# Kernel optimization log

Measured on AMD Instinct MI355X. Metric: run time of the kernel, lower is better.

The kernel has to match this reference:

```python
import jax, jax.numpy as jnp
import numpy as np

INPUT_DIM = 1024
OUTPUT_DIM = 1024
NUM_HEADS = 16  # NOTE: torch .split(num_heads) => chunk SIZE = num_heads
N_CHUNKS = OUTPUT_DIM // NUM_HEADS  # 64 effective heads of dim 16
NEG_INF = -1e9


def setup_inputs() -> dict:
    key = jax.random.key(0)
    k1, k2, k3, k4 = jax.random.split(key, 4)
    B, S = 32, 256
    x = jax.random.normal(k1, (B, S, INPUT_DIM), dtype=jnp.float32)
    mask = jnp.ones((B, S), dtype=jnp.float32)
    # xavier-uniform-ish linear weights, torch layout [out, in]
    lim = float(np.sqrt(6.0 / (INPUT_DIM + OUTPUT_DIM)))
    Wq = jax.random.uniform(k2, (OUTPUT_DIM, INPUT_DIM), jnp.float32, -lim, lim)
    Wk = jax.random.uniform(k3, (OUTPUT_DIM, INPUT_DIM), jnp.float32, -lim, lim)
    Wv = jax.random.uniform(k4, (OUTPUT_DIM, INPUT_DIM), jnp.float32, -lim, lim)
    return {"batch_sequence": x, "sequence_mask": mask, "Wq": Wq, "Wk": Wk, "Wv": Wv}


def _split_heads(m):
    # [B,S,D] -> chunks of size NUM_HEADS stacked in dim 0: [C,B,S,H]
    B, S, D = m.shape
    return jnp.transpose(m.reshape(B, S, N_CHUNKS, NUM_HEADS), (2, 0, 1, 3))


def reference(batch_sequence, sequence_mask, Wq, Wk, Wv):
    q = _split_heads(batch_sequence @ Wq.T)  # [C,B,S,H]
    k = _split_heads(batch_sequence @ Wk.T)
    v = _split_heads(batch_sequence @ Wv.T)
    logits = jnp.einsum("cbqh,cbkh->cbqk", q, k) / jnp.sqrt(
        jnp.asarray(OUTPUT_DIM, batch_sequence.dtype)
    )
    mask2d = sequence_mask[:, :, None] * sequence_mask[:, None, :]  # [B,S,S]
    logits = jnp.where(mask2d[None] > 0, logits, NEG_INF)
    w = jax.nn.softmax(logits, axis=-1)
    out = jnp.einsum("cbqk,cbkh->cbqh", w, v)  # [C,B,S,H]
    B, S = batch_sequence.shape[:2]
    return jnp.transpose(out, (1, 2, 0, 3)).reshape(B, S, OUTPUT_DIM)
```

## Files before the change

### kernel.cpp

```cpp
#include <hip/hip_runtime.h>


typedef unsigned short u16;
typedef unsigned int u32;
typedef __attribute__((ext_vector_type(8))) short short8;
typedef __attribute__((ext_vector_type(4))) short short4v;
typedef __attribute__((ext_vector_type(4))) float floatx4;

#if __has_builtin(__builtin_amdgcn_mfma_f32_16x16x16bf16_1k)
#define MFMA16(A, B, C) __builtin_amdgcn_mfma_f32_16x16x16bf16_1k(A, B, C, 0, 0, 0)
#elif __has_builtin(__builtin_amdgcn_mfma_f32_16x16x16_bf16)
#define MFMA16(A, B, C) __builtin_amdgcn_mfma_f32_16x16x16_bf16(A, B, C, 0, 0, 0)
#else
__device__ __forceinline__ floatx4 mfma16_asm(short4v a, short4v b, floatx4 c) {
  floatx4 d;
  asm volatile("v_mfma_f32_16x16x16_bf16 %0, %1, %2, %3"
               : "=v"(d) : "v"(a), "v"(b), "v"(c));
  return d;
}
#define MFMA16(A, B, C) mfma16_asm(A, B, C)
#endif

#if __has_builtin(__builtin_amdgcn_exp2f)
#define EXP2(x) __builtin_amdgcn_exp2f(x)
#else
#define EXP2(x) __expf((x) * 0.6931471805599453f)
#endif

#define QSCALE 0.045084220f

__device__ __forceinline__ u16 f2bf(float f) {
  union { float f; u32 u; } x; x.f = f;
  u32 r = x.u + 0x7fffu + ((x.u >> 16) & 1u);
  return (u16)(r >> 16);
}
__device__ __forceinline__ float bf2f(u16 u) {
  union { u32 u; float f; } x; x.u = ((u32)u) << 16;
  return x.f;
}

__device__ __forceinline__ void gload16(const void* g, void* l) {
  typedef __attribute__((address_space(1))) const unsigned int gq;
  typedef __attribute__((address_space(3))) unsigned int lq;
  __builtin_amdgcn_global_load_lds((gq*)(size_t)g, (lq*)(size_t)l, 16, 0, 0);
}

#define GK 1024
#define QKS 20
#define VTS 264

__global__ __launch_bounds__(256) void cast_all(const float* __restrict__ x,
                                                const float* __restrict__ wq,
                                                const float* __restrict__ wk,
                                                const float* __restrict__ wv,
                                                u16* __restrict__ XB,
                                                u16* __restrict__ WB) {
  int bid = blockIdx.x;
  const float* src; u16* dst; int off;
  if (bid < 8192)       { src = x;  dst = XB;                 off = bid; }
  else if (bid < 9216)  { src = wq; dst = WB;                 off = bid - 8192; }
  else if (bid < 10240) { src = wk; dst = WB + 1024 * 1024;   off = bid - 9216; }
  else                  { src = wv; dst = WB + 2 * 1024 * 1024; off = bid - 10240; }
  int i = (off * 256 + threadIdx.x) * 4;
  float4 v = *(const float4*)(src + i);
  u32 lo = (u32)f2bf(v.x) | ((u32)f2bf(v.y) << 16);
  u32 hi = (u32)f2bf(v.z) | ((u32)f2bf(v.w) << 16);
  uint2 o; o.x = lo; o.y = hi;
  *(uint2*)(dst + i) = o;
}

template <bool MASKED>
__device__ __forceinline__ void attn_loop2(const u16* __restrict__ Ks,
                                           const u16* __restrict__ Vt,
                                           const short4v* bq, const float* mqv,
                                           const float* m_s,
                                           floatx4* oacc, floatx4* lacc,
                                           int col, int quad) {
  const short4v ones = {(short)0x3F80, (short)0x3F80, (short)0x3F80, (short)0x3F80};
#pragma unroll 4
  for (int kt = 0; kt < 16; kt++) {
    const int kb = kt * 16;
    short4v ak = *(const short4v*)(Ks + (kb + col) * QKS + quad * 4);
    short4v av = *(const short4v*)(Vt + col * VTS + kb + quad * 4);
    float mk[4];
    if (MASKED) {
#pragma unroll
      for (int i = 0; i < 4; i++) mk[i] = m_s[kb + quad * 4 + i];
    }
#pragma unroll
    for (int qt = 0; qt < 2; qt++) {
      floatx4 z = {0.f, 0.f, 0.f, 0.f};
      floatx4 st = MFMA16(ak, bq[qt], z);
      float e[4];
#pragma unroll
      for (int i = 0; i < 4; i++) {
        e[i] = EXP2(st[i]);
        if (MASKED) e[i] = (mqv[qt] * mk[i] > 0.f) ? e[i] : 0.f;
      }
      union { u32 u[2]; short4v s; } pk;
      pk.u[0] = __builtin_amdgcn_perm(__float_as_uint(e[1]), __float_as_uint(e[0]), 0x07060302u);
      pk.u[1] = __builtin_amdgcn_perm(__float_as_uint(e[3]), __float_as_uint(e[2]), 0x07060302u);
      lacc[qt] = MFMA16(ones, pk.s, lacc[qt]);
      oacc[qt] = MFMA16(av, pk.s, oacc[qt]);
    }
  }
}

__global__ __launch_bounds__(512, 4) void fused_qkv_attn(const u16* __restrict__ XB,
                                                         const u16* __restrict__ WB,
                                                         const float* __restrict__ mask,
                                                         float* __restrict__ out) {
  __shared__ __align__(16) u16 smem[22528];
  __shared__ float m_s[256];

  const int bid = blockIdx.x;
  const int b = bid & 31;
  const int c0 = (bid >> 5) * 2;
  const int t = threadIdx.x;
  const int wave = t >> 6;
  const int lane = t & 63;
  const int col = lane & 15;
  const int quad = lane >> 4;

  u16* const Xs0 = smem;
  u16* const Xs1 = smem + 8192;
  u16* const Ws0 = smem + 16384;
  u16* const Ws1 = smem + 19456;

  float mv = (t < 256) ? mask[b * 256 + t] : 1.0f;
  if (t < 256) m_s[t] = mv;
  const int allones = __syncthreads_and(mv > 0.f);

  const int rl = lane >> 2;
  const int ch = lane & 3;
  const int sch = ch ^ ((rl >> 1) & 3);

  const size_t xsrc = ((size_t)b * 256 + wave * 32 + rl) * GK + sch * 8;
  const int xdst = wave * 1024;

  size_t wsrc = 0;
  if (wave < 6)
    wsrc = ((size_t)((wave % 3) * 1024 + (c0 + wave / 3) * 16 + rl)) * GK + sch * 8;
  const int wdst = wave * 512;

  floatx4 acc[2][6] = {};

  const int rpos = (quad ^ ((col >> 1) & 3)) * 8;
  const int arow0 = (wave * 32 + col) * 32 + rpos;

  gload16(XB + xsrc, Xs0 + xdst);
  gload16(XB + xsrc + (size_t)16 * GK, Xs0 + xdst + 512);
  if (wave < 6) gload16(WB + wsrc, Ws0 + wdst);

  auto gemm_step = [&](int knext, const u16* Xc, const u16* Wc, u16* Xn, u16* Wn) {
    if (knext >= 0) {
      gload16(XB + xsrc + knext, Xn + xdst);
      gload16(XB + xsrc + (size_t)16 * GK + knext, Xn + xdst + 512);
      if (wave < 6) {
        gload16(WB + wsrc + knext, Wn + wdst);
        asm volatile("s_waitcnt vmcnt(3)" ::: "memory");
      } else {
        asm volatile("s_waitcnt vmcnt(2)" ::: "memory");
      }
    } else {
      asm volatile("s_waitcnt vmcnt(0)" ::: "memory");
    }
    __builtin_amdgcn_sched_barrier(0);
    __builtin_amdgcn_s_barrier();
    __builtin_amdgcn_sched_barrier(0);

    short8 af[2], bf[6];
#pragma unroll
    for (int mt = 0; mt < 2; mt++)
      af[mt] = *(const short8*)(Xc + arow0 + mt * 512);
#pragma unroll
    for (int nt = 0; nt < 6; nt++)
      bf[nt] = *(const short8*)(Wc + (nt * 16 + col) * 32 + rpos);
#pragma unroll
    for (int mt = 0; mt < 2; mt++)
#pragma unroll
      for (int nt = 0; nt < 6; nt++)
        acc[mt][nt] = __builtin_amdgcn_mfma_f32_16x16x32_bf16(af[mt], bf[nt], acc[mt][nt], 0, 0, 0);

    asm volatile("s_waitcnt lgkmcnt(0)" ::: "memory");
    __builtin_amdgcn_sched_barrier(0);
    __builtin_amdgcn_s_barrier();
  };

#pragma unroll 1
  for (int tp = 0; tp < 15; tp++) {
    gemm_step((2 * tp + 1) * 32, Xs0, Ws0, Xs1, Ws1);
    gemm_step((2 * tp + 2) * 32, Xs1, Ws1, Xs0, Ws0);
  }
  gemm_step(31 * 32, Xs0, Ws0, Xs1, Ws1);
  gemm_step(-1, Xs1, Ws1, Xs0, Ws0);

  u16* const Qs = smem;
  u16* const Ks = smem + 5120;
  u16* const Vt = smem + 10240;
  float* const l_s = (float*)(smem + 14464);
  float* const ot = (float*)smem;

#pragma unroll
  for (int h = 0; h < 2; h++) {
    __syncthreads();

#pragma unroll
    for (int mt = 0; mt < 2; mt++) {
      const int row = wave * 32 + mt * 16 + quad * 4;
#pragma unroll
      for (int r = 0; r < 4; r++) {
        Qs[(row + r) * QKS + col] = f2bf(acc[mt][3 * h + 0][r] * QSCALE);
        Ks[(row + r) * QKS + col] = f2bf(acc[mt][3 * h + 1][r]);
        Vt[col * VTS + row + r] = f2bf(acc[mt][3 * h + 2][r]);
      }
    }
    __syncthreads();

    const int q0 = wave * 32;
    short4v bq[2];
    float mqv[2];
#pragma unroll
    for (int qt = 0; qt < 2; qt++) {
      bq[qt] = *(const short4v*)(Qs + (q0 + qt * 16 + col) * QKS + quad * 4);
      mqv[qt] = m_s[q0 + qt * 16 + col];
    }

    floatx4 oacc[2] = {};
    floatx4 lacc[2] = {};
    if (allones)
      attn_loop2<false>(Ks, Vt, bq, mqv, m_s, oacc, lacc, col, quad);
    else
      attn_loop2<true>(Ks, Vt, bq, mqv, m_s, oacc, lacc, col, quad);

    __syncthreads();
#pragma unroll
    for (int qt = 0; qt < 2; qt++) {
      if (quad == 0) l_s[q0 + qt * 16 + col] = lacc[qt][0];
#pragma unroll
      for (int r = 0; r < 4; r++)
        ot[(quad * 4 + r) * 257 + q0 + qt * 16 + col] = oacc[qt][r];
    }
    __syncthreads();

    const int row = t >> 1;
    const int hb = (t & 1) * 8;
    float l = l_s[row];
    float* op = out + ((size_t)b * 256 + row) * 1024 + (c0 + h) * 16 + hb;
    float o[8];
    if (allones || l > 0.f) {
      float inv = 1.0f / l;
#pragma unroll
      for (int j = 0; j < 8; j++) o[j] = ot[(hb + j) * 257 + row] * inv;
    } else {
#pragma unroll
      for (int j = 0; j < 8; j++) o[j] = 0.f;
      for (int k = 0; k < 256; k++)
#pragma unroll
        for (int j = 0; j < 8; j++) o[j] += bf2f(Vt[(hb + j) * VTS + k]);
#pragma unroll
      for (int j = 0; j < 8; j++) o[j] *= (1.0f / 256.0f);
    }
#pragma unroll
    for (int g = 0; g < 2; g++) {
      float4 r;
      r.x = o[g * 4 + 0]; r.y = o[g * 4 + 1]; r.z = o[g * 4 + 2]; r.w = o[g * 4 + 3];
      *(float4*)(op + g * 4) = r;
    }
  }
}

extern "C" void kernel_launch(void* const* d_in, const int* in_sizes, int n_in,
                              void* d_out, int out_size, void* d_ws, size_t ws_size,
                              hipStream_t stream) {
  const float* x    = (const float*)d_in[0];
  const float* mask = (const float*)d_in[1];
  const float* Wq   = (const float*)d_in[2];
  const float* Wk   = (const float*)d_in[3];
  const float* Wv   = (const float*)d_in[4];
  float* out = (float*)d_out;

  u16* XB = (u16*)d_ws;
  u16* WB = XB + (size_t)8192 * 1024;

  cast_all<<<11264, 256, 0, stream>>>(x, Wq, Wk, Wv, XB, WB);
  fused_qkv_attn<<<1024, 512, 0, stream>>>(XB, WB, mask, out);
}
```

Measured before the change: 167.5 us.

## Fuse x bf16 cast into attention GEMM and process four heads per block

Drops the separate pass that cast x to bf16. The fused kernel now loads fp32 x straight from global memory, converts it in registers with v_cvt_pk_bf16_f32, and writes it to LDS, so x is no longer written and re-read as bf16 through a workspace. Blocks grow to 1024 threads and handle four heads each, which halves the grid and halves how many times x is re-read across head groups. The waves are re-tiled 4x4 over rows and weights, and each wave now handles 16 queries in the attention phase. The trade-offs are register-staged x loads that are only partly overlapped with the MFMAs, more LDS, and a larger block that may lower occupancy.

```diff
diff --git a/kernel.cpp b/kernel.cpp
--- a/kernel.cpp
+++ b/kernel.cpp
@@ -39,6 +39,12 @@
   return x.f;
 }
 
+__device__ __forceinline__ u32 pkbf(float lo, float hi) {
+  u32 d;
+  asm("v_cvt_pk_bf16_f32 %0, %1, %2" : "=v"(d) : "v"(lo), "v"(hi));
+  return d;
+}
+
 __device__ __forceinline__ void gload16(const void* g, void* l) {
   typedef __attribute__((address_space(1))) const unsigned int gq;
   typedef __attribute__((address_space(3))) unsigned int lq;
@@ -49,32 +55,27 @@
 #define QKS 20
 #define VTS 264
 
-__global__ __launch_bounds__(256) void cast_all(const float* __restrict__ x,
-                                                const float* __restrict__ wq,
-                                                const float* __restrict__ wk,
-                                                const float* __restrict__ wv,
-                                                u16* __restrict__ XB,
-                                                u16* __restrict__ WB) {
+__global__ __launch_bounds__(256) void cast_w(const float* __restrict__ wq,
+                                              const float* __restrict__ wk,
+                                              const float* __restrict__ wv,
+                                              u16* __restrict__ WB) {
   int bid = blockIdx.x;
-  const float* src; u16* dst; int off;
-  if (bid < 8192)       { src = x;  dst = XB;                 off = bid; }
-  else if (bid < 9216)  { src = wq; dst = WB;                 off = bid - 8192; }
-  else if (bid < 10240) { src = wk; dst = WB + 1024 * 1024;   off = bid - 9216; }
-  else                  { src = wv; dst = WB + 2 * 1024 * 1024; off = bid - 10240; }
-  int i = (off * 256 + threadIdx.x) * 4;
+  const float* src = (bid < 1024) ? wq : (bid < 2048) ? wk : wv;
+  int seg = bid >> 10;
+  int i = ((bid & 1023) * 256 + threadIdx.x) * 4;
   float4 v = *(const float4*)(src + i);
-  u32 lo = (u32)f2bf(v.x) | ((u32)f2bf(v.y) << 16);
-  u32 hi = (u32)f2bf(v.z) | ((u32)f2bf(v.w) << 16);
-  uint2 o; o.x = lo; o.y = hi;
-  *(uint2*)(dst + i) = o;
+  uint2 o;
+  o.x = pkbf(v.x, v.y);
+  o.y = pkbf(v.z, v.w);
+  *(uint2*)(WB + (size_t)seg * 1024 * 1024 + i) = o;
 }
 
 template <bool MASKED>
-__device__ __forceinline__ void attn_loop2(const u16* __restrict__ Ks,
+__device__ __forceinline__ void attn_loop1(const u16* __restrict__ Ks,
                                            const u16* __restrict__ Vt,
-                                           const short4v* bq, const float* mqv,
+                                           short4v bq, float mqv,
                                            const float* m_s,
-                                           floatx4* oacc, floatx4* lacc,
+                                           floatx4& oacc, floatx4& lacc,
                                            int col, int quad) {
   const short4v ones = {(short)0x3F80, (short)0x3F80, (short)0x3F80, (short)0x3F80};
 #pragma unroll 4
@@ -82,118 +83,125 @@
     const int kb = kt * 16;
     short4v ak = *(const short4v*)(Ks + (kb + col) * QKS + quad * 4);
     short4v av = *(const short4v*)(Vt + col * VTS + kb + quad * 4);
-    float mk[4];
-    if (MASKED) {
-#pragma unroll
-      for (int i = 0; i < 4; i++) mk[i] = m_s[kb + quad * 4 + i];
-    }
-#pragma unroll
-    for (int qt = 0; qt < 2; qt++) {
-      floatx4 z = {0.f, 0.f, 0.f, 0.f};
-      floatx4 st = MFMA16(ak, bq[qt], z);
-      float e[4];
-#pragma unroll
-      for (int i = 0; i < 4; i++) {
-        e[i] = EXP2(st[i]);
-        if (MASKED) e[i] = (mqv[qt] * mk[i] > 0.f) ? e[i] : 0.f;
-      }
-      union { u32 u[2]; short4v s; } pk;
-      pk.u[0] = __builtin_amdgcn_perm(__float_as_uint(e[1]), __float_as_uint(e[0]), 0x07060302u);
-      pk.u[1] = __builtin_amdgcn_perm(__float_as_uint(e[3]), __float_as_uint(e[2]), 0x07060302u);
-      lacc[qt] = MFMA16(ones, pk.s, lacc[qt]);
-      oacc[qt] = MFMA16(av, pk.s, oacc[qt]);
-    }
-  }
-}
-
-__global__ __launch_bounds__(512, 4) void fused_qkv_attn(const u16* __restrict__ XB,
-                                                         const u16* __restrict__ WB,
-                                                         const float* __restrict__ mask,
-                                                         float* __restrict__ out) {
-  __shared__ __align__(16) u16 smem[22528];
+    floatx4 z = {0.f, 0.f, 0.f, 0.f};
+    floatx4 st = MFMA16(ak, bq, z);
+    float e[4];
+#pragma unroll
+    for (int i = 0; i < 4; i++) {
+      e[i] = EXP2(st[i]);
+      if (MASKED) e[i] = (mqv * m_s[kb + quad * 4 + i] > 0.f) ? e[i] : 0.f;
+    }
+    union { u32 u[2]; short4v s; } pk;
+    pk.u[0] = __builtin_amdgcn_perm(__float_as_uint(e[1]), __float_as_uint(e[0]), 0x07060302u);
+    pk.u[1] = __builtin_amdgcn_perm(__float_as_uint(e[3]), __float_as_uint(e[2]), 0x07060302u);
+    lacc = MFMA16(ones, pk.s, lacc);
+    oacc = MFMA16(av, pk.s, oacc);
+  }
+}
+
+__global__ __launch_bounds__(1024, 4) void fused_qkv_attn(const float* __restrict__ x,
+                                                          const u16* __restrict__ WB,
+                                                          const float* __restrict__ mask,
+                                                          float* __restrict__ out) {
+  __shared__ __align__(16) u16 smem[28672];
   __shared__ float m_s[256];
 
   const int bid = blockIdx.x;
   const int b = bid & 31;
-  const int c0 = (bid >> 5) * 2;
+  const int c0 = (bid >> 5) * 4;
   const int t = threadIdx.x;
   const int wave = t >> 6;
   const int lane = t & 63;
   const int col = lane & 15;
   const int quad = lane >> 4;
+  const int wm = wave & 3;
+  const int wn = wave >> 2;
 
   u16* const Xs0 = smem;
   u16* const Xs1 = smem + 8192;
-  u16* const Ws0 = smem + 16384;
-  u16* const Ws1 = smem + 19456;
+  u16* const WsA = smem + 16384;
+  u16* const WsB = smem + 22528;
 
   float mv = (t < 256) ? mask[b * 256 + t] : 1.0f;
   if (t < 256) m_s[t] = mv;
   const int allones = __syncthreads_and(mv > 0.f);
 
-  const int rl = lane >> 2;
-  const int ch = lane & 3;
-  const int sch = ch ^ ((rl >> 1) & 3);
-
-  const size_t xsrc = ((size_t)b * 256 + wave * 32 + rl) * GK + sch * 8;
-  const int xdst = wave * 1024;
-
+  const int xr = t >> 2;
+  const int xch = t & 3;
+  const float* const xg = x + ((size_t)b * 256 + xr) * GK + xch * 8;
+  const int xdst = xr * 32 + (xch ^ ((xr >> 1) & 3)) * 8;
+
+  const int wr = lane >> 2;
+  const int wch = lane & 3;
+  const int wsch = wch ^ ((wr >> 1) & 3);
   size_t wsrc = 0;
-  if (wave < 6)
-    wsrc = ((size_t)((wave % 3) * 1024 + (c0 + wave / 3) * 16 + rl)) * GK + sch * 8;
+  if (wave < 12) {
+    const int mat = wave % 3, head = wave / 3;
+    wsrc = ((size_t)(mat * 1024 + (c0 + head) * 16 + wr)) * GK + wsch * 8;
+  }
   const int wdst = wave * 512;
 
-  floatx4 acc[2][6] = {};
+  floatx4 acc[4][3] = {};
 
   const int rpos = (quad ^ ((col >> 1) & 3)) * 8;
-  const int arow0 = (wave * 32 + col) * 32 + rpos;
-
-  gload16(XB + xsrc, Xs0 + xdst);
-  gload16(XB + xsrc + (size_t)16 * GK, Xs0 + xdst + 512);
-  if (wave < 6) gload16(WB + wsrc, Ws0 + wdst);
+  const int abase = (wm * 64 + col) * 32 + rpos;
+  const int bbase = (wn * 48 + col) * 32 + rpos;
+
+  if (wave < 12) gload16(WB + wsrc, WsA + wdst);
+  {
+    float4 a0 = *(const float4*)(xg);
+    float4 a1 = *(const float4*)(xg + 4);
+    asm volatile("s_waitcnt vmcnt(0)" ::: "memory");
+    uint4 w;
+    w.x = pkbf(a0.x, a0.y); w.y = pkbf(a0.z, a0.w);
+    w.z = pkbf(a1.x, a1.y); w.w = pkbf(a1.z, a1.w);
+    *(uint4*)(Xs0 + xdst) = w;
+  }
+  asm volatile("s_waitcnt lgkmcnt(0)" ::: "memory");
+  __builtin_amdgcn_sched_barrier(0);
+  __builtin_amdgcn_s_barrier();
+  __builtin_amdgcn_sched_barrier(0);
 
   auto gemm_step = [&](int knext, const u16* Xc, const u16* Wc, u16* Xn, u16* Wn) {
+    float4 a0, a1;
     if (knext >= 0) {
-      gload16(XB + xsrc + knext, Xn + xdst);
-      gload16(XB + xsrc + (size_t)16 * GK + knext, Xn + xdst + 512);
-      if (wave < 6) {
-        gload16(WB + wsrc + knext, Wn + wdst);
-        asm volatile("s_waitcnt vmcnt(3)" ::: "memory");
-      } else {
-        asm volatile("s_waitcnt vmcnt(2)" ::: "memory");
-      }
-    } else {
+      if (wave < 12) gload16(WB + wsrc + knext, Wn + wdst);
+      a0 = *(const float4*)(xg + knext);
+      a1 = *(const float4*)(xg + knext + 4);
+    }
+    __builtin_amdgcn_sched_barrier(0);
+
+    short8 af[4], bf[3];
+#pragma unroll
+    for (int mt = 0; mt < 4; mt++)
+      af[mt] = *(const short8*)(Xc + abase + mt * 512);
+#pragma unroll
+    for (int n = 0; n < 3; n++)
+      bf[n] = *(const short8*)(Wc + bbase + n * 512);
+#pragma unroll
+    for (int mt = 0; mt < 4; mt++)
+#pragma unroll
+      for (int n = 0; n < 3; n++)
+        acc[mt][n] = __builtin_amdgcn_mfma_f32_16x16x32_bf16(af[mt], bf[n], acc[mt][n], 0, 0, 0);
+
+    if (knext >= 0) {
       asm volatile("s_waitcnt vmcnt(0)" ::: "memory");
-    }
+      uint4 w;
+      w.x = pkbf(a0.x, a0.y); w.y = pkbf(a0.z, a0.w);
+      w.z = pkbf(a1.x, a1.y); w.w = pkbf(a1.z, a1.w);
+      *(uint4*)(Xn + xdst) = w;
+    }
+    asm volatile("s_waitcnt lgkmcnt(0)" ::: "memory");
     __builtin_amdgcn_sched_barrier(0);
     __builtin_amdgcn_s_barrier();
     __builtin_amdgcn_sched_barrier(0);
-
-    short8 af[2], bf[6];
-#pragma unroll
-    for (int mt = 0; mt < 2; mt++)
-      af[mt] = *(const short8*)(Xc + arow0 + mt * 512);
-#pragma unroll
-    for (int nt = 0; nt < 6; nt++)
-      bf[nt] = *(const short8*)(Wc + (nt * 16 + col) * 32 + rpos);
-#pragma unroll
-    for (int mt = 0; mt < 2; mt++)
-#pragma unroll
-      for (int nt = 0; nt < 6; nt++)
-        acc[mt][nt] = __builtin_amdgcn_mfma_f32_16x16x32_bf16(af[mt], bf[nt], acc[mt][nt], 0, 0, 0);
-
-    asm volatile("s_waitcnt lgkmcnt(0)" ::: "memory");
-    __builtin_amdgcn_sched_barrier(0);
-    __builtin_amdgcn_s_barrier();
   };
 
 #pragma unroll 1
-  for (int tp = 0; tp < 15; tp++) {
-    gemm_step((2 * tp + 1) * 32, Xs0, Ws0, Xs1, Ws1);
-    gemm_step((2 * tp + 2) * 32, Xs1, Ws1, Xs0, Ws0);
-  }
-  gemm_step(31 * 32, Xs0, Ws0, Xs1, Ws1);
-  gemm_step(-1, Xs1, Ws1, Xs0, Ws0);
+  for (int tp = 0; tp < 16; tp++) {
+    gemm_step((2 * tp + 1) * 32, Xs0, WsA, Xs1, WsB);
+    gemm_step((tp == 15) ? -1 : (2 * tp + 2) * 32, Xs1, WsB, Xs0, WsA);
+  }
 
   u16* const Qs = smem;
   u16* const Ks = smem + 5120;
@@ -202,71 +210,61 @@
   float* const ot = (float*)smem;
 
 #pragma unroll
-  for (int h = 0; h < 2; h++) {
-    __syncthreads();
-
-#pragma unroll
-    for (int mt = 0; mt < 2; mt++) {
-      const int row = wave * 32 + mt * 16 + quad * 4;
-#pragma unroll
-      for (int r = 0; r < 4; r++) {
-        Qs[(row + r) * QKS + col] = f2bf(acc[mt][3 * h + 0][r] * QSCALE);
-        Ks[(row + r) * QKS + col] = f2bf(acc[mt][3 * h + 1][r]);
-        Vt[col * VTS + row + r] = f2bf(acc[mt][3 * h + 2][r]);
+  for (int h = 0; h < 4; h++) {
+    __syncthreads();
+
+    if (wn == h) {
+#pragma unroll
+      for (int mt = 0; mt < 4; mt++) {
+        const int row = wm * 64 + mt * 16 + quad * 4;
+#pragma unroll
+        for (int r = 0; r < 4; r++) {
+          Qs[(row + r) * QKS + col] = f2bf(acc[mt][0][r] * QSCALE);
+          Ks[(row + r) * QKS + col] = f2bf(acc[mt][1][r]);
+          Vt[col * VTS + row + r] = f2bf(acc[mt][2][r]);
+        }
       }
     }
     __syncthreads();
 
-    const int q0 = wave * 32;
-    short4v bq[2];
-    float mqv[2];
-#pragma unroll
-    for (int qt = 0; qt < 2; qt++) {
-      bq[qt] = *(const short4v*)(Qs + (q0 + qt * 16 + col) * QKS + quad * 4);
-      mqv[qt] = m_s[q0 + qt * 16 + col];
-    }
-
-    floatx4 oacc[2] = {};
-    floatx4 lacc[2] = {};
+    const int q0 = wave * 16;
+    short4v bq = *(const short4v*)(Qs + (q0 + col) * QKS + quad * 4);
+    float mqv = m_s[q0 + col];
+    floatx4 oacc = {};
+    floatx4 lacc = {};
     if (allones)
-      attn_loop2<false>(Ks, Vt, bq, mqv, m_s, oacc, lacc, col, quad);
+      attn_loop1<false>(Ks, Vt, bq, mqv, m_s, oacc, lacc, col, quad);
     else
-      attn_loop2<true>(Ks, Vt, bq, mqv, m_s, oacc, lacc, col, quad);
-
-    __syncthreads();
-#pragma unroll
-    for (int qt = 0; qt < 2; qt++) {
-      if (quad == 0) l_s[q0 + qt * 16 + col] = lacc[qt][0];
-#pragma unroll
-      for (int r = 0; r < 4; r++)
-        ot[(quad * 4 + r) * 257 + q0 + qt * 16 + col] = oacc[qt][r];
-    }
-    __syncthreads();
-
-    const int row = t >> 1;
-    const int hb = (t & 1) * 8;
+      attn_loop1<true>(Ks, Vt, bq, mqv, m_s, oacc, lacc, col, quad);
+
+    __syncthreads();
+    if (quad == 0) l_s[q0 + col] = lacc[0];
+#pragma unroll
+    for (int r = 0; r < 4; r++)
+      ot[(quad * 4 + r) * 257 + q0 + col] = oacc[r];
+    __syncthreads();
+
+    const int row = t >> 2;
+    const int hb = (t & 3) * 4;
     float l = l_s[row];
     float* op = out + ((size_t)b * 256 + row) * 1024 + (c0 + h) * 16 + hb;
-    float o[8];
+    float o[4];
     if (allones || l > 0.f) {
       float inv = 1.0f / l;
 #pragma unroll
-      for (int j = 0; j < 8; j++) o[j] = ot[(hb + j) * 257 + row] * inv;
+      for (int j = 0; j < 4; j++) o[j] = ot[(hb + j) * 257 + row] * inv;
     } else {
 #pragma unroll
-      for (int j = 0; j < 8; j++) o[j] = 0.f;
+      for (int j = 0; j < 4; j++) o[j] = 0.f;
       for (int k = 0; k < 256; k++)
 #pragma unroll
-        for (int j = 0; j < 8; j++) o[j] += bf2f(Vt[(hb + j) * VTS + k]);
-#pragma unroll
-      for (int j = 0; j < 8; j++) o[j] *= (1.0f / 256.0f);
-    }
-#pragma unroll
-    for (int g = 0; g < 2; g++) {
-      float4 r;
-      r.x = o[g * 4 + 0]; r.y = o[g * 4 + 1]; r.z = o[g * 4 + 2]; r.w = o[g * 4 + 3];
-      *(float4*)(op + g * 4) = r;
-    }
+        for (int j = 0; j < 4; j++) o[j] += bf2f(Vt[(hb + j) * VTS + k]);
+#pragma unroll
+      for (int j = 0; j < 4; j++) o[j] *= (1.0f / 256.0f);
+    }
+    float4 rr;
+    rr.x = o[0]; rr.y = o[1]; rr.z = o[2]; rr.w = o[3];
+    *(float4*)op = rr;
   }
 }
 
@@ -280,9 +278,8 @@
   const float* Wv   = (const float*)d_in[4];
   float* out = (float*)d_out;
 
-  u16* XB = (u16*)d_ws;
-  u16* WB = XB + (size_t)8192 * 1024;
-
-  cast_all<<<11264, 256, 0, stream>>>(x, Wq, Wk, Wv, XB, WB);
-  fused_qkv_attn<<<1024, 512, 0, stream>>>(XB, WB, mask, out);
-}
+  u16* WB = (u16*)d_ws;
+
+  cast_w<<<3072, 256, 0, stream>>>(Wq, Wk, Wv, WB);
+  fused_qkv_attn<<<512, 1024, 0, stream>>>(x, WB, mask, out);
+}
```

Result: slower. 192.8 us (+15.1%).
